# Optimization experiments

Hardware: AMD Instinct MI355X
Metric: run time of the kernel (lower is better)

Reference implementation:

```python
import jax, jax.numpy as jnp
import numpy as np

H = 512          # hidden_size
SF = 4           # scale_factor
B, S, L = 16, 2048, 2

def setup_inputs() -> dict:
    key = jax.random.key(0)
    ks = jax.random.split(key, 9)
    return {
        "hidden": jax.random.normal(ks[0], (L, B, H * SF), dtype=jnp.float32),
        "encoder_outputs": jax.random.normal(ks[1], (B, S, H * SF), dtype=jnp.float32),
        "We": jax.random.normal(ks[2], (H, H * SF), dtype=jnp.float32) * 0.02,
        "be": jax.random.normal(ks[3], (H,), dtype=jnp.float32) * 0.02,
        "Wh": jax.random.normal(ks[4], (H, H * SF), dtype=jnp.float32) * 0.02,
        "bh": jax.random.normal(ks[5], (H,), dtype=jnp.float32) * 0.02,
        "Wa": jax.random.normal(ks[6], (H, 2 * H), dtype=jnp.float32) * 0.02,
        "ba": jax.random.normal(ks[7], (H,), dtype=jnp.float32) * 0.02,
        "v": jax.random.uniform(ks[8], (1, H), dtype=jnp.float32),
    }

def reference(hidden, encoder_outputs, We, be, Wh, bh, Wa, ba, v):
    # hidden[-1]: [B, 4H] -> [B, H]
    h = hidden[-1] @ Wh.T + bh
    # encoder_outputs: [B, S, 4H] -> [B, S, H]
    eo = jnp.einsum('bsf,hf->bsh', encoder_outputs, We) + be
    # concat([h broadcast to S, eo]) @ Wa.T == h @ Wa_h.T + eo @ Wa_e.T (split concat matmul)
    Wa_h, Wa_e = Wa[:, :H], Wa[:, H:]
    energy = jnp.tanh(h[:, None, :] @ Wa_h.T + jnp.einsum('bsh,kh->bsk', eo, Wa_e) + ba)  # [B,S,H]
    scores = jnp.einsum('bsh,h->bs', energy, v[0])           # [B,S]
    attn_weights = jax.nn.softmax(scores, axis=1)            # [B,S]
    context_vector = jnp.einsum('bs,bsh->bh', attn_weights, eo)  # [B,H]
    return (context_vector, attn_weights)
```

## Files before the change

kernel.cpp:

```cpp
#include <hip/hip_runtime.h>
#include <math.h>

#define HH 512
#define FF 2048
#define BB 16
#define SS 2048
#define MM 32768

using f32x4 = __attribute__((ext_vector_type(4))) float;
using s16x8 = __attribute__((ext_vector_type(8))) short;

struct __align__(8)  US4 { unsigned short x, y, z, w; };
struct __align__(16) US8 { unsigned short s[8]; };

__device__ __forceinline__ unsigned short f2bf(float f) {
  unsigned int u = __builtin_bit_cast(unsigned int, f);
  u += 0x7fffu + ((u >> 16) & 1u);
  return (unsigned short)(u >> 16);
}
__device__ __forceinline__ float bf2f(unsigned short u) {
  unsigned int x = ((unsigned int)u) << 16;
  return __builtin_bit_cast(float, x);
}
__device__ __forceinline__ void gload_lds16(const void* g, void* l) {
  __builtin_amdgcn_global_load_lds(
      (const __attribute__((address_space(1))) unsigned int*)g,
      (__attribute__((address_space(3))) unsigned int*)l, 16, 0, 0);
}

__global__ void k_conv(const float* __restrict__ We, const float* __restrict__ Wa,
                       unsigned short* __restrict__ OWe, unsigned short* __restrict__ OWa) {
  int bid = blockIdx.x, t = threadIdx.x;
  if (bid < 1024) {
    int idx = bid * 256 + t;
    f32x4 x = *(const f32x4*)(We + (size_t)idx * 4);
    US4 p{f2bf(x.x), f2bf(x.y), f2bf(x.z), f2bf(x.w)};
    *(US4*)(OWe + (size_t)idx * 4) = p;
  } else {
    int idx = (bid - 1024) * 256 + t;
    int k = idx >> 7, h4 = idx & 127;
    f32x4 x = *(const f32x4*)(Wa + (size_t)k * 1024 + 512 + h4 * 4);
    US4 p{f2bf(x.x), f2bf(x.y), f2bf(x.z), f2bf(x.w)};
    *(US4*)(OWa + (size_t)idx * 4) = p;
  }
}

__global__ void k_h(const float* __restrict__ hidden, const float* __restrict__ Wh,
                    const float* __restrict__ bh, float* __restrict__ h_ws) {
  int t = threadIdx.x, lane = t & 63, wid = t >> 6;
  int out = blockIdx.x * 4 + wid;
  int b = out >> 9, j = out & 511;
  const float* hr = hidden + (1) * BB * FF + b * FF;
  const float* wr = Wh + (size_t)j * FF;
  float a = 0.f;
#pragma unroll
  for (int i = 0; i < 8; ++i) {
    int o = i * 256 + lane * 4;
    f32x4 x = *(const f32x4*)(hr + o);
    f32x4 y = *(const f32x4*)(wr + o);
    a += x.x * y.x + x.y * y.y + x.z * y.z + x.w * y.w;
  }
#pragma unroll
  for (int m = 32; m; m >>= 1) a += __shfl_xor(a, m);
  if (lane == 0) h_ws[out] = a + bh[j];
}

__global__ void k_bb(const float* __restrict__ h_ws, const float* __restrict__ Wa,
                     const float* __restrict__ ba, float* __restrict__ bb_ws) {
  int t = threadIdx.x, lane = t & 63, wid = t >> 6;
  int out = blockIdx.x * 4 + wid;
  int b = out >> 9, k = out & 511;
  const float* hr = h_ws + b * HH;
  const float* wa = Wa + (size_t)k * 1024;
  float a = 0.f;
#pragma unroll
  for (int i = 0; i < 2; ++i) {
    int o = i * 256 + lane * 4;
    f32x4 x = *(const f32x4*)(hr + o);
    f32x4 y = *(const f32x4*)(wa + o);
    a += x.x * y.x + x.y * y.y + x.z * y.z + x.w * y.w;
  }
#pragma unroll
  for (int m = 32; m; m >>= 1) a += __shfl_xor(a, m);
  if (lane == 0) bb_ws[out] = a + ba[k];
}

__global__ __launch_bounds__(512, 4) void k_gemm1f(
    const float* __restrict__ enc, const unsigned short* __restrict__ Web,
    const float* __restrict__ be, const unsigned short* __restrict__ Waeb,
    const float* __restrict__ bbw, const float* __restrict__ vv,
    unsigned short* __restrict__ eo, float* __restrict__ sp) {
  __shared__ unsigned short smem[36864];
  unsigned short* As = smem;
  unsigned short* Bs = smem + 4096;
  const int t = threadIdx.x, lane = t & 63, wid = t >> 6;
  const int m0 = blockIdx.x * 64;
  const float* enc_m0 = enc + (size_t)m0 * FF;
  f32x4 acc[4][4] = {};

  f32x4 areg[2];
#pragma unroll
  for (int i = 0; i < 2; ++i) {
    int idx = i * 512 + t, row = idx >> 4, c4 = idx & 15;
    areg[i] = *(const f32x4*)(enc_m0 + (size_t)row * FF + c4 * 4);
  }

#pragma unroll 1
  for (int kt = 0; kt < FF; kt += 64) {
#pragma unroll
    for (int i = 0; i < 8; ++i) {
      int idx = i * 512 + t, row = idx >> 3, c = idx & 7, sc = c ^ (row & 7);
      gload_lds16(Web + (size_t)row * FF + kt + sc * 8, Bs + idx * 8);
    }
#pragma unroll
    for (int i = 0; i < 2; ++i) {
      int idx = i * 512 + t, row = idx >> 4, c4 = idx & 15;
      f32x4 x = areg[i];
      US4 p{f2bf(x.x), f2bf(x.y), f2bf(x.z), f2bf(x.w)};
      int byte = row * 128 + ((c4 * 8) ^ ((row & 7) << 4));
      *(US4*)((char*)As + byte) = p;
    }
    {
      int ktn = (kt + 64 < FF) ? kt + 64 : 0;
#pragma unroll
      for (int i = 0; i < 2; ++i) {
        int idx = i * 512 + t, row = idx >> 4, c4 = idx & 15;
        areg[i] = *(const f32x4*)(enc_m0 + (size_t)row * FF + ktn + c4 * 4);
      }
    }
    asm volatile("s_waitcnt vmcnt(2) lgkmcnt(0)" ::: "memory");
    __builtin_amdgcn_s_barrier();
    __builtin_amdgcn_sched_barrier(0);
#pragma unroll
    for (int ks = 0; ks < 2; ++ks) {
      s16x8 af[4], bfr[4];
#pragma unroll
      for (int mi = 0; mi < 4; ++mi) {
        int row = mi * 16 + (lane & 15);
        int byte = row * 128 + (((ks * 64) + (lane >> 4) * 16) ^ ((row & 7) << 4));
        af[mi] = *(const s16x8*)((const char*)As + byte);
      }
#pragma unroll
      for (int ni = 0; ni < 4; ++ni) {
        int row = wid * 64 + ni * 16 + (lane & 15);
        int byte = row * 128 + (((ks * 64) + (lane >> 4) * 16) ^ ((row & 7) << 4));
        bfr[ni] = *(const s16x8*)((const char*)Bs + byte);
      }
#pragma unroll
      for (int mi = 0; mi < 4; ++mi)
#pragma unroll
        for (int ni = 0; ni < 4; ++ni)
          acc[mi][ni] = __builtin_amdgcn_mfma_f32_16x16x32_bf16(af[mi], bfr[ni], acc[mi][ni], 0, 0, 0);
    }
    asm volatile("s_waitcnt lgkmcnt(0)" ::: "memory");
    __builtin_amdgcn_s_barrier();
    __builtin_amdgcn_sched_barrier(0);
  }

  unsigned short* Cs = smem + 4096;
#pragma unroll
  for (int ni = 0; ni < 4; ++ni) {
    int col = wid * 64 + ni * 16 + (lane & 15);
    float bev = be[col];
#pragma unroll
    for (int mi = 0; mi < 4; ++mi)
#pragma unroll
      for (int j = 0; j < 4; ++j) {
        int row = mi * 16 + (lane >> 4) * 4 + j;
        int byte = row * 1024 + ((col * 2) ^ ((row & 7) << 4));
        *(unsigned short*)((char*)Cs + byte) = f2bf(acc[mi][ni][j] + bev);
      }
  }
  __syncthreads();

#pragma unroll
  for (int i = 0; i < 8; ++i) {
    int idx = i * 512 + t, row = idx >> 6, c = idx & 63;
    int byte = row * 1024 + ((c * 16) ^ ((row & 7) << 4));
    *(US8*)(eo + (size_t)(m0 + row) * HH + c * 8) = *(const US8*)((const char*)Cs + byte);
  }

  f32x4 acc2[4][4] = {};
#pragma unroll
  for (int kt2 = 0; kt2 < HH; kt2 += 64) {
#pragma unroll
    for (int ks = 0; ks < 2; ++ks) {
      int k2 = kt2 + ks * 32 + (lane >> 4) * 8;
      s16x8 af[4], bfr[4];
#pragma unroll
      for (int mi = 0; mi < 4; ++mi) {
        int row = mi * 16 + (lane & 15);
        int byte = row * 1024 + ((k2 * 2) ^ ((row & 7) << 4));
        af[mi] = *(const s16x8*)((const char*)Cs + byte);
      }
#pragma unroll
      for (int ni = 0; ni < 4; ++ni) {
        int nrow = wid * 64 + ni * 16 + (lane & 15);
        bfr[ni] = *(const s16x8*)(Waeb + (size_t)nrow * HH + k2);
      }
#pragma unroll
      for (int mi = 0; mi < 4; ++mi)
#pragma unroll
        for (int ni = 0; ni < 4; ++ni)
          acc2[mi][ni] = __builtin_amdgcn_mfma_f32_16x16x32_bf16(af[mi], bfr[ni], acc2[mi][ni], 0, 0, 0);
    }
  }

  const int b = m0 >> 11;
  float vcol[4], bcol[4];
#pragma unroll
  for (int ni = 0; ni < 4; ++ni) {
    int col = wid * 64 + ni * 16 + (lane & 15);
    vcol[ni] = vv[col];
    bcol[ni] = bbw[b * HH + col];
  }
  float ps[4][4];
#pragma unroll
  for (int mi = 0; mi < 4; ++mi)
#pragma unroll
    for (int j = 0; j < 4; ++j) {
      float s = 0.f;
#pragma unroll
      for (int ni = 0; ni < 4; ++ni)
        s += tanhf(acc2[mi][ni][j] + bcol[ni]) * vcol[ni];
      ps[mi][j] = s;
    }
#pragma unroll
  for (int m = 1; m < 16; m <<= 1)
#pragma unroll
    for (int mi = 0; mi < 4; ++mi)
#pragma unroll
      for (int j = 0; j < 4; ++j) ps[mi][j] += __shfl_xor(ps[mi][j], m);
  float* red = (float*)smem;
  if ((lane & 15) == 0) {
#pragma unroll
    for (int mi = 0; mi < 4; ++mi)
#pragma unroll
      for (int j = 0; j < 4; ++j)
        red[wid * 64 + mi * 16 + (lane >> 4) * 4 + j] = ps[mi][j];
  }
  __syncthreads();
  if (t < 64) {
    float s = 0.f;
#pragma unroll
    for (int w = 0; w < 8; ++w) s += red[w * 64 + t];
    sp[m0 + t] = s;
  }
}

__global__ void k_softmax(const float* __restrict__ sp, float* __restrict__ attn) {
  const int b = blockIdx.x, t = threadIdx.x, lane = t & 63, wid = t >> 6;
  __shared__ float red[4];
  float vals[8], lmax = -3.0e38f;
#pragma unroll
  for (int i = 0; i < 8; ++i) {
    float x = sp[b * SS + t + i * 256];
    vals[i] = x;
    lmax = fmaxf(lmax, x);
  }
#pragma unroll
  for (int m = 32; m; m >>= 1) lmax = fmaxf(lmax, __shfl_xor(lmax, m));
  if (lane == 0) red[wid] = lmax;
  __syncthreads();
  lmax = fmaxf(fmaxf(red[0], red[1]), fmaxf(red[2], red[3]));
  __syncthreads();
  float lsum = 0.f;
#pragma unroll
  for (int i = 0; i < 8; ++i) {
    vals[i] = __expf(vals[i] - lmax);
    lsum += vals[i];
  }
#pragma unroll
  for (int m = 32; m; m >>= 1) lsum += __shfl_xor(lsum, m);
  if (lane == 0) red[wid] = lsum;
  __syncthreads();
  float inv = 1.0f / (red[0] + red[1] + red[2] + red[3]);
#pragma unroll
  for (int i = 0; i < 8; ++i) attn[b * SS + t + i * 256] = vals[i] * inv;
}

__global__ __launch_bounds__(512) void k_ctx1(const unsigned short* __restrict__ eo,
                                              const float* __restrict__ attn,
                                              float* __restrict__ cp) {
  __shared__ float red[8][512];
  const int b = blockIdx.x >> 4, ch = blockIdx.x & 15, t = threadIdx.x;
  const int tg = t & 63, sg = t >> 6;
  const float* aw = attn + b * SS + ch * 128;
  float acc[8] = {};
#pragma unroll 4
  for (int i = 0; i < 16; ++i) {
    int s = sg + i * 8;
    float w = aw[s];
    US8 vv8 = *(const US8*)(eo + (size_t)(b * SS + ch * 128 + s) * HH + tg * 8);
#pragma unroll
    for (int j = 0; j < 8; ++j) acc[j] += w * bf2f(vv8.s[j]);
  }
#pragma unroll
  for (int j = 0; j < 8; ++j) red[sg][tg * 8 + j] = acc[j];
  __syncthreads();
  float a = 0.f;
#pragma unroll
  for (int g = 0; g < 8; ++g) a += red[g][t];
  cp[(size_t)blockIdx.x * HH + t] = a;
}

__global__ void k_ctx2(const float* __restrict__ cp, float* __restrict__ ctx) {
  const int b = blockIdx.x, h = threadIdx.x;
  float a = 0.f;
#pragma unroll
  for (int c = 0; c < 16; ++c) a += cp[(size_t)(b * 16 + c) * HH + h];
  ctx[b * HH + h] = a;
}

extern "C" void kernel_launch(void* const* d_in, const int* in_sizes, int n_in,
                              void* d_out, int out_size, void* d_ws, size_t ws_size,
                              hipStream_t stream) {
  (void)in_sizes; (void)n_in; (void)out_size; (void)ws_size;
  const float* hidden = (const float*)d_in[0];
  const float* enc    = (const float*)d_in[1];
  const float* We     = (const float*)d_in[2];
  const float* be     = (const float*)d_in[3];
  const float* Wh     = (const float*)d_in[4];
  const float* bh     = (const float*)d_in[5];
  const float* Wa     = (const float*)d_in[6];
  const float* ba     = (const float*)d_in[7];
  const float* v      = (const float*)d_in[8];

  float* out  = (float*)d_out;
  float* ctx  = out;
  float* attn = out + BB * HH;

  char* ws = (char*)d_ws;
  unsigned short* Web  = (unsigned short*)ws;  ws += (size_t)HH * FF * 2;
  unsigned short* Waeb = (unsigned short*)ws;  ws += (size_t)HH * HH * 2;
  float* h_ws  = (float*)ws;                   ws += (size_t)BB * HH * 4;
  float* bb_ws = (float*)ws;                   ws += (size_t)BB * HH * 4;
  unsigned short* eo = (unsigned short*)ws;    ws += (size_t)MM * HH * 2;
  float* sp = (float*)ws;                      ws += (size_t)MM * 4;
  float* cp = (float*)ws;                      ws += (size_t)BB * 16 * HH * 4;

  k_conv<<<1280, 256, 0, stream>>>(We, Wa, Web, Waeb);
  k_h<<<2048, 256, 0, stream>>>(hidden, Wh, bh, h_ws);
  k_bb<<<2048, 256, 0, stream>>>(h_ws, Wa, ba, bb_ws);
  k_gemm1f<<<512, 512, 0, stream>>>(enc, Web, be, Waeb, bb_ws, v, eo, sp);
  k_softmax<<<16, 256, 0, stream>>>(sp, attn);
  k_ctx1<<<256, 512, 0, stream>>>(eo, attn, cp);
  k_ctx2<<<16, 512, 0, stream>>>(cp, ctx);
}
```

Before: 170.5 us.

## Merge weight-convert and hidden projection kernels, stagger GEMM K start, raise MFMA priority

Folds the bf16 weight conversion and the hidden-state projection into one launch, removing a kernel launch and its serialization gap. In the main GEMM, odd blocks start their K loop halfway through the reduction dimension, so concurrent blocks read different columns of the shared weight matrix and contend less on the same cache lines and channels. The MFMA section is wrapped in s_setprio to favour compute waves over load-issuing waves. These are three unrelated tweaks; the K rotation changes the summation order slightly.

```diff
diff --git a/kernel.cpp b/kernel.cpp
--- a/kernel.cpp
+++ b/kernel.cpp
@@ -28,41 +28,41 @@
       (__attribute__((address_space(3))) unsigned int*)l, 16, 0, 0);
 }
 
-__global__ void k_conv(const float* __restrict__ We, const float* __restrict__ Wa,
-                       unsigned short* __restrict__ OWe, unsigned short* __restrict__ OWa) {
+__global__ void k_prep(const float* __restrict__ We, const float* __restrict__ Wa,
+                       const float* __restrict__ hidden, const float* __restrict__ Wh,
+                       const float* __restrict__ bh,
+                       unsigned short* __restrict__ OWe, unsigned short* __restrict__ OWa,
+                       float* __restrict__ h_ws) {
   int bid = blockIdx.x, t = threadIdx.x;
   if (bid < 1024) {
     int idx = bid * 256 + t;
     f32x4 x = *(const f32x4*)(We + (size_t)idx * 4);
     US4 p{f2bf(x.x), f2bf(x.y), f2bf(x.z), f2bf(x.w)};
     *(US4*)(OWe + (size_t)idx * 4) = p;
-  } else {
+  } else if (bid < 1280) {
     int idx = (bid - 1024) * 256 + t;
     int k = idx >> 7, h4 = idx & 127;
     f32x4 x = *(const f32x4*)(Wa + (size_t)k * 1024 + 512 + h4 * 4);
     US4 p{f2bf(x.x), f2bf(x.y), f2bf(x.z), f2bf(x.w)};
     *(US4*)(OWa + (size_t)idx * 4) = p;
-  }
-}
-
-__global__ void k_h(const float* __restrict__ hidden, const float* __restrict__ Wh,
-                    const float* __restrict__ bh, float* __restrict__ h_ws) {
-  int t = threadIdx.x, lane = t & 63, wid = t >> 6;
-  int out = blockIdx.x * 4 + wid;
-  int b = out >> 9, j = out & 511;
-  const float* hr = hidden + (1) * BB * FF + b * FF;
-  const float* wr = Wh + (size_t)j * FF;
-  float a = 0.f;
-#pragma unroll
-  for (int i = 0; i < 8; ++i) {
-    int o = i * 256 + lane * 4;
-    f32x4 x = *(const f32x4*)(hr + o);
-    f32x4 y = *(const f32x4*)(wr + o);
-    a += x.x * y.x + x.y * y.y + x.z * y.z + x.w * y.w;
-  }
-#pragma unroll
-  for (int m = 32; m; m >>= 1) a += __shfl_xor(a, m);
-  if (lane == 0) h_ws[out] = a + bh[j];
+  } else {
+    int lane = t & 63, wid = t >> 6;
+    int out = (bid - 1280) * 4 + wid;
+    int b = out >> 9, j = out & 511;
+    const float* hr = hidden + (1) * BB * FF + b * FF;
+    const float* wr = Wh + (size_t)j * FF;
+    float a = 0.f;
+#pragma unroll
+    for (int i = 0; i < 8; ++i) {
+      int o = i * 256 + lane * 4;
+      f32x4 x = *(const f32x4*)(hr + o);
+      f32x4 y = *(const f32x4*)(wr + o);
+      a += x.x * y.x + x.y * y.y + x.z * y.z + x.w * y.w;
+    }
+#pragma unroll
+    for (int m = 32; m; m >>= 1) a += __shfl_xor(a, m);
+    if (lane == 0) h_ws[out] = a + bh[j];
+  }
 }
 
 __global__ void k_bb(const float* __restrict__ h_ws, const float* __restrict__ Wa,
@@ -95,6 +95,7 @@
   unsigned short* Bs = smem + 4096;
   const int t = threadIdx.x, lane = t & 63, wid = t >> 6;
   const int m0 = blockIdx.x * 64;
+  const int koff = (blockIdx.x & 1) << 10;
   const float* enc_m0 = enc + (size_t)m0 * FF;
   f32x4 acc[4][4] = {};
 
@@ -102,15 +103,17 @@
 #pragma unroll
   for (int i = 0; i < 2; ++i) {
     int idx = i * 512 + t, row = idx >> 4, c4 = idx & 15;
-    areg[i] = *(const f32x4*)(enc_m0 + (size_t)row * FF + c4 * 4);
+    areg[i] = *(const f32x4*)(enc_m0 + (size_t)row * FF + koff + c4 * 4);
   }
 
 #pragma unroll 1
   for (int kt = 0; kt < FF; kt += 64) {
+    const int kc = (kt + koff) & 2047;
+    const int kn = (kt + 64 + koff) & 2047;
 #pragma unroll
     for (int i = 0; i < 8; ++i) {
       int idx = i * 512 + t, row = idx >> 3, c = idx & 7, sc = c ^ (row & 7);
-      gload_lds16(Web + (size_t)row * FF + kt + sc * 8, Bs + idx * 8);
+      gload_lds16(Web + (size_t)row * FF + kc + sc * 8, Bs + idx * 8);
     }
 #pragma unroll
     for (int i = 0; i < 2; ++i) {
@@ -120,17 +123,15 @@
       int byte = row * 128 + ((c4 * 8) ^ ((row & 7) << 4));
       *(US4*)((char*)As + byte) = p;
     }
-    {
-      int ktn = (kt + 64 < FF) ? kt + 64 : 0;
-#pragma unroll
-      for (int i = 0; i < 2; ++i) {
-        int idx = i * 512 + t, row = idx >> 4, c4 = idx & 15;
-        areg[i] = *(const f32x4*)(enc_m0 + (size_t)row * FF + ktn + c4 * 4);
-      }
+#pragma unroll
+    for (int i = 0; i < 2; ++i) {
+      int idx = i * 512 + t, row = idx >> 4, c4 = idx & 15;
+      areg[i] = *(const f32x4*)(enc_m0 + (size_t)row * FF + kn + c4 * 4);
     }
     asm volatile("s_waitcnt vmcnt(2) lgkmcnt(0)" ::: "memory");
     __builtin_amdgcn_s_barrier();
     __builtin_amdgcn_sched_barrier(0);
+    __builtin_amdgcn_s_setprio(1);
 #pragma unroll
     for (int ks = 0; ks < 2; ++ks) {
       s16x8 af[4], bfr[4];
@@ -152,6 +153,7 @@
         for (int ni = 0; ni < 4; ++ni)
           acc[mi][ni] = __builtin_amdgcn_mfma_f32_16x16x32_bf16(af[mi], bfr[ni], acc[mi][ni], 0, 0, 0);
     }
+    __builtin_amdgcn_s_setprio(0);
     asm volatile("s_waitcnt lgkmcnt(0)" ::: "memory");
     __builtin_amdgcn_s_barrier();
     __builtin_amdgcn_sched_barrier(0);
@@ -339,8 +341,7 @@
   float* sp = (float*)ws;                      ws += (size_t)MM * 4;
   float* cp = (float*)ws;                      ws += (size_t)BB * 16 * HH * 4;
 
-  k_conv<<<1280, 256, 0, stream>>>(We, Wa, Web, Waeb);
-  k_h<<<2048, 256, 0, stream>>>(hidden, Wh, bh, h_ws);
+  k_prep<<<3328, 256, 0, stream>>>(We, Wa, hidden, Wh, bh, Web, Waeb, h_ws);
   k_bb<<<2048, 256, 0, stream>>>(h_ws, Wa, ba, bb_ws);
   k_gemm1f<<<512, 512, 0, stream>>>(enc, Web, be, Waeb, bb_ws, v, eo, sp);
   k_softmax<<<16, 256, 0, stream>>>(sp, attn);
```

Result: slower. 239.7 us (+40.6%).
